# Optimization experiments

Hardware: AMD Instinct MI355X
Metric: run time of the kernel (lower is better)

Reference implementation:

```python
import jax, jax.numpy as jnp
import numpy as np

V = 1024      # token vocab
C = 8         # n_codebooks
T = 256       # seg_len
BP = 4        # block_pairs (n_latent_blocks)
K = 512       # latent_vocab_size (codebook entries)
E = 128       # emb_dim
D = 128       # latent_dim / d_model
BETA = 0.05
NB = 6 * BP   # decoder sequence length = 24
NH = 4
HD = D // NH
FF = 512
R = 8
IN_FLAT = NB * D
OUT = T * C * V
B = 32


def setup_inputs() -> dict:
    key = jax.random.key(0)
    ks = jax.random.split(key, 20)
    n = lambda i, shape, s=0.02: jax.random.normal(ks[i], shape, jnp.float32) * s
    return {
        "tokens_prev": jax.random.randint(ks[0], (B, T, C), 0, V, jnp.int32),
        "tokens_curr": jax.random.randint(ks[1], (B, T, C), 0, V, jnp.int32),
        "tokens_next": jax.random.randint(ks[2], (B, T, C), 0, V, jnp.int32),
        "emb": n(3, (V, E)),
        "conv1_w": n(4, (4 * D, E * C, 3)),
        "conv1_b": jnp.zeros((4 * D,), jnp.float32),
        "conv2_w": n(5, (2 * D, 4 * D, 1)),
        "conv2_b": jnp.zeros((2 * D,), jnp.float32),
        "cb_instru": jax.random.uniform(ks[6], (K, D), jnp.float32, -1.0 / K, 1.0 / K),
        "cb_vocal": jax.random.uniform(ks[7], (K, D), jnp.float32, -1.0 / K, 1.0 / K),
        "pos": n(8, (1, NB, D), 1.0),
        "attn_in_w": n(9, (3 * D, D)),
        "attn_in_b": jnp.zeros((3 * D,), jnp.float32),
        "attn_out_w": n(10, (D, D)),
        "attn_out_b": jnp.zeros((D,), jnp.float32),
        "ln1_g": jnp.ones((D,), jnp.float32),
        "ln1_b": jnp.zeros((D,), jnp.float32),
        "lin1_w": n(11, (FF, D)),
        "lin1_b": jnp.zeros((FF,), jnp.float32),
        "lin2_w": n(12, (D, FF)),
        "lin2_b": jnp.zeros((D,), jnp.float32),
        "ln2_g": jnp.ones((D,), jnp.float32),
        "ln2_b": jnp.zeros((D,), jnp.float32),
        "lora_a": n(13, (R, IN_FLAT), 0.01),
        "lora_b": n(14, (OUT, R), 0.01),
    }


def _conv1d(x, w, b, pad):
    # x: (B, Cin, L), w: (Cout, Cin, Kw)
    y = jax.lax.conv_general_dilated(x, w, window_strides=(1,), padding=[(pad, pad)],
                                     dimension_numbers=("NCH", "OIH", "NCH"))
    return y + b[None, :, None]


def _encode(tokens, emb, w1, b1, w2, b2):
    Bb, Tt, Cc = tokens.shape
    x = emb[tokens].reshape(Bb, Tt, -1).transpose(0, 2, 1)       # (B, C*E, T)
    x = jax.nn.relu(_conv1d(x, w1, b1, 1))                        # (B, 4D, T)
    x = jax.nn.relu(_conv1d(x, w2, b2, 0))                        # (B, 2D, T)
    # AdaptiveAvgPool1d(BP) with T % BP == 0 -> mean over contiguous chunks
    x = x.reshape(Bb, 2 * D, BP, Tt // BP).mean(-1).transpose(0, 2, 1)  # (B, BP, 2D)
    return x[..., :D], x[..., D:]


def _vq(z, codebook):
    # z: (B, N, D); eval-mode VQ (no EMA update)
    Bb, N, Dd = z.shape
    flat = z.reshape(-1, Dd)
    dist = (jnp.sum(flat * flat, axis=1, keepdims=True)
            - 2.0 * flat @ codebook.T
            + jnp.sum(codebook * codebook, axis=1))
    codes = jnp.argmin(dist, axis=1)
    z_q = codebook[codes].reshape(Bb, N, Dd)
    commit = jnp.mean((z - jax.lax.stop_gradient(z_q)) ** 2)
    loss = BETA * commit
    z_q_st = z + jax.lax.stop_gradient(z_q - z)
    return z_q_st, codes.reshape(Bb, N), loss


def _layer_norm(x, g, b):
    mu = x.mean(-1, keepdims=True)
    var = ((x - mu) ** 2).mean(-1, keepdims=True)
    return (x - mu) * jax.lax.rsqrt(var + 1e-5) * g + b


def _tf_layer(x, in_w, in_b, out_w, out_b, g1, b1, w1, bb1, w2, bb2, g2, b2):
    # Post-norm TransformerEncoderLayer (relu, eval/no-dropout). x: (B, S, D)
    Bb, S, Dd = x.shape
    qkv = x @ in_w.T + in_b
    q, k, v = jnp.split(qkv, 3, axis=-1)
    q = q.reshape(Bb, S, NH, HD).transpose(0, 2, 1, 3)
    k = k.reshape(Bb, S, NH, HD).transpose(0, 2, 1, 3)
    v = v.reshape(Bb, S, NH, HD).transpose(0, 2, 1, 3)
    attn = jax.nn.softmax(jnp.einsum("bhsd,bhtd->bhst", q, k) / np.sqrt(HD), axis=-1)
    o = jnp.einsum("bhst,bhtd->bhsd", attn, v).transpose(0, 2, 1, 3).reshape(Bb, S, Dd)
    x = _layer_norm(x + o @ out_w.T + out_b, g1, b1)
    ff = jax.nn.relu(x @ w1.T + bb1) @ w2.T + bb2
    return _layer_norm(x + ff, g2, b2)


def reference(tokens_prev, tokens_curr, tokens_next, emb, conv1_w, conv1_b,
              conv2_w, conv2_b, cb_instru, cb_vocal, pos, attn_in_w, attn_in_b,
              attn_out_w, attn_out_b, ln1_g, ln1_b, lin1_w, lin1_b, lin2_w,
              lin2_b, ln2_g, ln2_b, lora_a, lora_b):
    p_i, p_v = _encode(tokens_prev, emb, conv1_w, conv1_b, conv2_w, conv2_b)
    c_i, c_v = _encode(tokens_curr, emb, conv1_w, conv1_b, conv2_w, conv2_b)
    n_i, n_v = _encode(tokens_next, emb, conv1_w, conv1_b, conv2_w, conv2_b)
    p_i_q, _, l1 = _vq(p_i, cb_instru)
    c_i_q, _, l2 = _vq(c_i, cb_instru)
    n_i_q, _, l3 = _vq(n_i, cb_instru)
    p_v_q, _, l4 = _vq(p_v, cb_vocal)
    c_v_q, _, l5 = _vq(c_v, cb_vocal)
    n_v_q, _, l6 = _vq(n_v, cb_vocal)
    vq_loss = l1 + l2 + l3 + l4 + l5 + l6
    z = jnp.concatenate([p_i_q, p_v_q, c_i_q, c_v_q, n_i_q, n_v_q], axis=1)  # (B, 24, D)
    z = z + pos[:, :z.shape[1], :]
    z = _tf_layer(z, attn_in_w, attn_in_b, attn_out_w, attn_out_b,
                  ln1_g, ln1_b, lin1_w, lin1_b, lin2_w, lin2_b, ln2_g, ln2_b)
    Bb = z.shape[0]
    flat = z.reshape(Bb, -1)
    logits = (flat @ lora_a.T) @ lora_b.T          # (B, T*C*V)
    logits = logits.reshape(Bb, T, C, V)
    logp = jax.nn.log_softmax(logits, axis=-1)
    nll = -jnp.take_along_axis(logp, tokens_curr[..., None].astype(jnp.int32), axis=-1)
    recon_loss = nll.mean()
    total_loss = recon_loss + vq_loss
    return total_loss
```

## Files before the change

kernel.cpp:

```cpp
#include <hip/hip_runtime.h>
#include <hip/hip_bf16.h>
#include <cstdint>
#include <cstddef>

typedef __attribute__((ext_vector_type(8))) short short8;
typedef __attribute__((ext_vector_type(4))) float floatx4;


__device__ __forceinline__ ushort f2bf(float f) {
    union { float f; unsigned int u; } x; x.f = f;
    unsigned int r = (x.u + 0x7fffu + ((x.u >> 16) & 1u)) >> 16;
    return (ushort)r;
}
__device__ __forceinline__ float bf2f(ushort u) {
    union { unsigned int u; float f; } x; x.u = ((unsigned int)u) << 16;
    return x.f;
}

__global__ __launch_bounds__(256) void prep_all(
    const float* __restrict__ emb, const float* __restrict__ w1,
    const float* __restrict__ w2, const float* __restrict__ cbi,
    const float* __restrict__ cbv, const float* __restrict__ aiw,
    const float* __restrict__ aow, const float* __restrict__ l1w,
    const float* __restrict__ l2w,
    ushort* __restrict__ ebf, ushort* __restrict__ w1bf, ushort* __restrict__ w2bf,
    float* __restrict__ cbiT, float* __restrict__ cbvT,
    ushort* __restrict__ aiwbf, ushort* __restrict__ aowbf,
    ushort* __restrict__ l1wbf, ushort* __restrict__ l2wbf,
    float* __restrict__ accum)
{
    int idx = blockIdx.x * 256 + threadIdx.x;
    if (idx < 16) accum[idx] = 0.f;
    if (idx < 131072) {
        ebf[idx] = f2bf(emb[idx]);
    } else if (idx < 262144) {
        int j = idx - 131072; w2bf[j] = f2bf(w2[j]);
    } else if (idx < 327680) {
        int j = idx - 262144; cbiT[(j & 127) * 512 + (j >> 7)] = cbi[j];
    } else if (idx < 393216) {
        int j = idx - 327680; cbvT[(j & 127) * 512 + (j >> 7)] = cbv[j];
    } else if (idx < 442368) {
        int j = idx - 393216; aiwbf[j] = f2bf(aiw[j]);
    } else if (idx < 475136) {
        int j = idx - 442368; aowbf[j] = f2bf(aow[j]);
    } else if (idx < 540672) {
        int j = idx - 475136; l1wbf[j] = f2bf(l1w[j]);
    } else if (idx < 606208) {
        int j = idx - 540672; l2wbf[j] = f2bf(l2w[j]);
    } else if (idx < 1130496) {
        int j = idx - 606208;
        int e  = j & 127;
        int cc = (j >> 7) & 7;
        int co = j >> 10;
        const float* src = w1 + ((size_t)co * 1024 + cc * 128 + e) * 3;
        float v0 = src[0], v1 = src[1], v2 = src[2];
        w1bf[((size_t)(0 * 8 + cc) * 512 + co) * 128 + e] = f2bf(v0);
        w1bf[((size_t)(1 * 8 + cc) * 512 + co) * 128 + e] = f2bf(v1);
        w1bf[((size_t)(2 * 8 + cc) * 512 + co) * 128 + e] = f2bf(v2);
    }
}

__global__ __launch_bounds__(512, 4) void conv1_mfma(
    const int* __restrict__ tp, const int* __restrict__ tcu, const int* __restrict__ tn,
    const ushort* __restrict__ ebf, const ushort* __restrict__ w1bf,
    const float* __restrict__ b1, ushort* __restrict__ y1)
{
    constexpr int LDA = 136;
    __shared__ ushort As[130 * LDA];
    __shared__ ushort Bs[128 * LDA];
    __shared__ int tokL[130 * 8];
    const int tid = threadIdx.x;
    const int bx = blockIdx.x;
    const int nb = bx & 3, mb = bx >> 2;
    const int set = mb >> 6, rem = mb & 63, bb = rem >> 1, t0 = (rem & 1) << 7;
    const int n0 = nb << 7;
    const int* tok = (set == 0) ? tp : ((set == 1) ? tcu : tn);

    for (int idx = tid; idx < 1040; idx += 512) {
        const int row = idx >> 3, cc = idx & 7;
        const int gt = t0 + row - 1;
        tokL[idx] = (gt >= 0 && gt < 256) ? tok[bb * 2048 + gt * 8 + cc] : -1;
    }

    const int w = tid >> 6, lane = tid & 63;
    const int wm = w & 1, wn = w >> 1;
    const int rA = lane & 15, q4 = lane >> 4;
    const int ch = tid & 15, rowst = tid >> 4;

    floatx4 acc[4][2];
    for (int mi = 0; mi < 4; ++mi)
        for (int ni = 0; ni < 2; ++ni)
            acc[mi][ni] = (floatx4)(0.0f);

    __syncthreads();

    for (int cc = 0; cc < 8; ++cc) {
        for (int p = 0; p < 5; ++p) {
            const int row = p * 32 + rowst;
            if (row < 130) {
                const int tk = tokL[row * 8 + cc];
                uint4 val = make_uint4(0u, 0u, 0u, 0u);
                if (tk >= 0) val = *(const uint4*)(ebf + tk * 128 + ch * 8);
                *(uint4*)(As + row * LDA + ch * 8) = val;
            }
        }
        for (int kw = 0; kw < 3; ++kw) {
            const ushort* wsrc = w1bf + ((size_t)((kw * 8 + cc) * 512 + n0)) * 128;
            for (int p = 0; p < 4; ++p) {
                const int row = p * 32 + rowst;
                *(uint4*)(Bs + row * LDA + ch * 8) = *(const uint4*)(wsrc + row * 128 + ch * 8);
            }
            __syncthreads();
            for (int ks = 0; ks < 4; ++ks) {
                const int k0 = ks * 32 + q4 * 8;
                short8 a[4], bfr[2];
                for (int mi = 0; mi < 4; ++mi)
                    a[mi] = *(const short8*)(As + (wm * 64 + mi * 16 + rA + kw) * LDA + k0);
                for (int ni = 0; ni < 2; ++ni)
                    bfr[ni] = *(const short8*)(Bs + (wn * 32 + ni * 16 + rA) * LDA + k0);
                for (int mi = 0; mi < 4; ++mi)
                    for (int ni = 0; ni < 2; ++ni)
                        acc[mi][ni] = __builtin_amdgcn_mfma_f32_16x16x32_bf16(
                            a[mi], bfr[ni], acc[mi][ni], 0, 0, 0);
            }
            __syncthreads();
        }
    }
    for (int ni = 0; ni < 2; ++ni) {
        const int co = n0 + wn * 32 + ni * 16 + rA;
        const float bias = b1[co];
        for (int mi = 0; mi < 4; ++mi) {
            for (int r = 0; r < 4; ++r) {
                const int t = t0 + wm * 64 + mi * 16 + q4 * 4 + r;
                float v = acc[mi][ni][r] + bias;
                v = v > 0.f ? v : 0.f;
                y1[((size_t)(set * 32 + bb) * 256 + t) * 512 + co] = f2bf(v);
            }
        }
    }
}

__global__ __launch_bounds__(512, 4) void conv2_mfma(
    const ushort* __restrict__ y1, const ushort* __restrict__ w2bf,
    const float* __restrict__ b2, float* __restrict__ y2)
{
    constexpr int LDA = 136;
    __shared__ ushort As[128 * LDA];
    __shared__ ushort Bs[128 * LDA];
    __shared__ float pool[256];
    const int tid = threadIdx.x;
    const int bx = blockIdx.x;
    const int nb = bx & 1, mb = bx >> 1;
    const int set = mb >> 6, rem = mb & 63, bb = rem >> 1, t0 = (rem & 1) << 7;
    const int n0 = nb << 7;
    const int w = tid >> 6, lane = tid & 63;
    const int wm = w & 1, wn = w >> 1;
    const int rA = lane & 15, q4 = lane >> 4;
    const int ch = tid & 15, rowst = tid >> 4;

    floatx4 acc[4][2];
    for (int mi = 0; mi < 4; ++mi)
        for (int ni = 0; ni < 2; ++ni)
            acc[mi][ni] = (floatx4)(0.0f);

    const size_t arowbase = ((size_t)(set * 32 + bb) * 256 + t0) * 512;
    for (int kc = 0; kc < 4; ++kc) {
        for (int p = 0; p < 4; ++p) {
            const int row = p * 32 + rowst;
            *(uint4*)(As + row * LDA + ch * 8) =
                *(const uint4*)(y1 + arowbase + (size_t)row * 512 + kc * 128 + ch * 8);
            *(uint4*)(Bs + row * LDA + ch * 8) =
                *(const uint4*)(w2bf + (size_t)(n0 + row) * 512 + kc * 128 + ch * 8);
        }
        __syncthreads();
        for (int ks = 0; ks < 4; ++ks) {
            const int k0 = ks * 32 + q4 * 8;
            short8 a[4], bfr[2];
            for (int mi = 0; mi < 4; ++mi)
                a[mi] = *(const short8*)(As + (wm * 64 + mi * 16 + rA) * LDA + k0);
            for (int ni = 0; ni < 2; ++ni)
                bfr[ni] = *(const short8*)(Bs + (wn * 32 + ni * 16 + rA) * LDA + k0);
            for (int mi = 0; mi < 4; ++mi)
                for (int ni = 0; ni < 2; ++ni)
                    acc[mi][ni] = __builtin_amdgcn_mfma_f32_16x16x32_bf16(
                        a[mi], bfr[ni], acc[mi][ni], 0, 0, 0);
        }
        __syncthreads();
    }
    for (int ni = 0; ni < 2; ++ni) {
        const int col = wn * 32 + ni * 16 + rA;
        const float bias = b2[n0 + col];
        float s = 0.f;
        for (int mi = 0; mi < 4; ++mi)
            for (int r = 0; r < 4; ++r) {
                float v = acc[mi][ni][r] + bias;
                s += v > 0.f ? v : 0.f;
            }
        s += __shfl_xor(s, 16);
        s += __shfl_xor(s, 32);
        if (q4 == 0) pool[wm * 128 + col] = s;
    }
    __syncthreads();
    if (tid < 256) {
        const int wrow = tid >> 7, col = tid & 127;
        const int p = (t0 >> 6) + wrow;
        y2[((size_t)(set * 32 + bb) * 4 + p) * 256 + n0 + col] = pool[tid] * (1.f / 64.f);
    }
}

__global__ __launch_bounds__(256) void vq_kernel(
    const float* __restrict__ y2, const float* __restrict__ cbiT, const float* __restrict__ cbvT,
    const float* __restrict__ cbi, const float* __restrict__ cbv,
    const float* __restrict__ pos, float* __restrict__ ztr, float* __restrict__ accum)
{
    const int q = blockIdx.x;
    const int tid = threadIdx.x;
    const int set = q >> 7, bb = (q >> 2) & 31, p = q & 3;
    __shared__ float zloc[256];
    __shared__ float bestv[4];
    __shared__ int   besti[4];
    __shared__ int   code_sh[2];
    __shared__ float wsum2[4];
    zloc[tid] = y2[(size_t)q * 256 + tid];
    __syncthreads();
    const int w = tid >> 6, lane = tid & 63;
    const int half = w >> 1, sub = w & 1;
    const float4* cbT4 = (const float4*)(half ? cbvT : cbiT);
    const float* zh = zloc + half * 128;
    const int k4 = sub * 64 + lane;
    float a0 = 0.f, a1 = 0.f, a2 = 0.f, a3 = 0.f;
    for (int d = 0; d < 128; ++d) {
        float4 v = cbT4[d * 128 + k4];
        const float z = zh[d];
        float d0 = z - v.x, d1 = z - v.y, d2 = z - v.z, d3 = z - v.w;
        a0 += d0 * d0; a1 += d1 * d1; a2 += d2 * d2; a3 += d3 * d3;
    }
    float best = a0; int bidx = k4 * 4;
    if (a1 < best) { best = a1; bidx = k4 * 4 + 1; }
    if (a2 < best) { best = a2; bidx = k4 * 4 + 2; }
    if (a3 < best) { best = a3; bidx = k4 * 4 + 3; }
    for (int off = 32; off > 0; off >>= 1) {
        float ov = __shfl_xor(best, off);
        int   oi = __shfl_xor(bidx, off);
        if (ov < best || (ov == best && oi < bidx)) { best = ov; bidx = oi; }
    }
    if (lane == 0) { bestv[w] = best; besti[w] = bidx; }
    __syncthreads();
    if (tid < 2) {
        float v0 = bestv[tid * 2], v1 = bestv[tid * 2 + 1];
        int   i0 = besti[tid * 2], i1 = besti[tid * 2 + 1];
        code_sh[tid] = (v1 < v0 || (v1 == v0 && i1 < i0)) ? i1 : i0;
    }
    __syncthreads();
    const int hh = tid >> 7, d = tid & 127;
    const int code = code_sh[hh];
    const float* cb = hh ? cbv : cbi;
    const float zq = cb[code * 128 + d];
    const float diff = zloc[hh * 128 + d] - zq;
    float sq = diff * diff;
    for (int off = 32; off > 0; off >>= 1) sq += __shfl_xor(sq, off);
    if (lane == 0) wsum2[w] = sq;
    const int s = (set * 2 + hh) * 4 + p;
    ztr[((size_t)bb * 24 + s) * 128 + d] = zq + pos[s * 128 + d];
    __syncthreads();
    if (tid == 0) atomicAdd(&accum[0], wsum2[0] + wsum2[1] + wsum2[2] + wsum2[3]);
}

__global__ __launch_bounds__(1024) void tail_kernel(
    const float* __restrict__ ztr,
    const ushort* __restrict__ aiwbf, const float* __restrict__ aib,
    const ushort* __restrict__ aowbf, const float* __restrict__ aob,
    const float* __restrict__ g1, const float* __restrict__ be1,
    const ushort* __restrict__ l1wbf, const float* __restrict__ l1b,
    const ushort* __restrict__ l2wbf, const float* __restrict__ l2b,
    const float* __restrict__ g2, const float* __restrict__ be2,
    const float* __restrict__ lora_a, float* __restrict__ hbuf)
{
    __shared__ __align__(16) char LDSC[162304];
    float*  Xf  = (float*)LDSC;
    ushort* Abf = (ushort*)(LDSC + 12288);
    char*   S   = LDSC + 20992;
    ushort* Wq  = (ushort*)S;
    float*  QKV = (float*)(S + 104448);
    float*  Ssc = (float*)S;
    ushort* Wo  = (ushort*)S;
    float*  psA = (float*)(S + 36864);
    float*  pqA = (float*)(S + 37888);
    float*  muvA= (float*)(S + 38912);
    float*  invA= (float*)(S + 39040);
    ushort* W1  = (ushort*)S;
    ushort* Hbf = (ushort*)S;
    ushort* Wh  = (ushort*)(S + 33280);
    float*  psB = (float*)(S + 100864);
    float*  pqB = (float*)(S + 101888);
    float*  muvB= (float*)(S + 102912);
    float*  invB= (float*)(S + 103040);
    float*  psL = (float*)(S + 103168);

    const int b = blockIdx.x;
    const int tid = threadIdx.x;
    const int w = tid >> 6, lane = tid & 63;
    const int rA = lane & 15, q4 = lane >> 4;
    const int ch = tid & 15;

    if (tid < 544) ((uint4*)Abf)[tid] = make_uint4(0u, 0u, 0u, 0u);
    __syncthreads();
    for (int i = tid; i < 3072; i += 1024) {
        float v = ztr[(size_t)b * 3072 + i];
        Xf[i] = v;
        Abf[(i >> 7) * 136 + (i & 127)] = f2bf(v);
    }
    for (int i = tid; i < 6144; i += 1024) {
        const int row = i >> 4, c = i & 15;
        *(uint4*)(Wq + row * 136 + c * 8) = *(const uint4*)(aiwbf + row * 128 + c * 8);
    }
    __syncthreads();

    {
        floatx4 acc[3];
        int mI[3], nI[3];
        for (int i = 0; i < 3; ++i) {
            const int t = w + 16 * i;
            mI[i] = t / 24; nI[i] = t % 24;
            acc[i] = (floatx4)(0.f);
        }
        for (int ks = 0; ks < 4; ++ks) {
            const int k0 = ks * 32 + q4 * 8;
            for (int i = 0; i < 3; ++i) {
                short8 a = *(const short8*)(Abf + (mI[i] * 16 + rA) * 136 + k0);
                short8 bf = *(const short8*)(Wq + (nI[i] * 16 + rA) * 136 + k0);
                acc[i] = __builtin_amdgcn_mfma_f32_16x16x32_bf16(a, bf, acc[i], 0, 0, 0);
            }
        }
        for (int i = 0; i < 3; ++i) {
            const int col = nI[i] * 16 + rA;
            const float bs = aib[col];
            for (int r = 0; r < 4; ++r) {
                const int row = mI[i] * 16 + q4 * 4 + r;
                if (row < 24) QKV[row * 384 + col] = acc[i][r] + bs;
            }
        }
    }
    __syncthreads();

    for (int it = 0; it < 3; ++it) {
        const int e = it * 1024 + tid;
        if (e < 2304) {
            const int h = e / 576, rem = e % 576, i = rem / 24, j = rem % 24;
            float s = 0.f;
            for (int d = 0; d < 32; ++d)
                s += QKV[i * 384 + h * 32 + d] * QKV[j * 384 + 128 + h * 32 + d];
            Ssc[h * 576 + i * 24 + j] = s * 0.17677669529663687f;
        }
    }
    __syncthreads();
    if (tid < 96) {
        const int h = tid / 24, r = tid % 24;
        float* row = Ssc + h * 576 + r * 24;
        float m = row[0];
        for (int j = 1; j < 24; ++j) m = row[j] > m ? row[j] : m;
        float ssum = 0.f;
        for (int j = 0; j < 24; ++j) { float e = __expf(row[j] - m); row[j] = e; ssum += e; }
        float iv = 1.f / ssum;
        for (int j = 0; j < 24; ++j) row[j] *= iv;
    }
    __syncthreads();
    for (int it = 0; it < 3; ++it) {
        const int idx = it * 1024 + tid;
        const int s = idx >> 7, dcol = idx & 127, h = dcol >> 5, d = dcol & 31;
        if (s < 24) {
            float a = 0.f;
            for (int j = 0; j < 24; ++j)
                a += Ssc[h * 576 + s * 24 + j] * QKV[j * 384 + 256 + h * 32 + d];
            Abf[s * 136 + dcol] = f2bf(a);
        }
    }
    __syncthreads();

    for (int i = tid; i < 2048; i += 1024) {
        const int row = i >> 4, c = i & 15;
        *(uint4*)(Wo + row * 136 + c * 8) = *(const uint4*)(aowbf + row * 128 + c * 8);
    }
    __syncthreads();

    {
        const int m = w & 1, n = w >> 1;
        floatx4 acc = (floatx4)(0.f);
        for (int ks = 0; ks < 4; ++ks) {
            const int k0 = ks * 32 + q4 * 8;
            short8 a = *(const short8*)(Abf + (m * 16 + rA) * 136 + k0);
            short8 bf = *(const short8*)(Wo + (n * 16 + rA) * 136 + k0);
            acc = __builtin_amdgcn_mfma_f32_16x16x32_bf16(a, bf, acc, 0, 0, 0);
        }
        const int col = n * 16 + rA;
        const float bs = aob[col];
        for (int r = 0; r < 4; ++r) {
            const int row = m * 16 + q4 * 4 + r;
            acc[r] += bs + (row < 24 ? Xf[row * 128 + col] : 0.f);
        }
        float s4 = 0.f, q4s = 0.f;
        for (int r = 0; r < 4; ++r) {
            float s = acc[r], sq = acc[r] * acc[r];
            for (int off = 1; off < 16; off <<= 1) { s += __shfl_xor(s, off); sq += __shfl_xor(sq, off); }
            if (rA == 0) {
                const int rl = m * 16 + q4 * 4 + r;
                psA[rl * 8 + n] = s; pqA[rl * 8 + n] = sq;
            }
        }
        (void)s4; (void)q4s;
        __syncthreads();
        if (tid < 32) {
            float s = 0.f, sq = 0.f;
            for (int j = 0; j < 8; ++j) { s += psA[tid * 8 + j]; sq += pqA[tid * 8 + j]; }
            float mu = s * (1.f / 128.f);
            float var = sq * (1.f / 128.f) - mu * mu;
            muvA[tid] = mu; invA[tid] = rsqrtf(var + 1e-5f);
        }
        __syncthreads();
        const float gg = g1[col], bb2 = be1[col];
        for (int r = 0; r < 4; ++r) {
            const int rl = m * 16 + q4 * 4 + r;
            if (rl < 24) {
                float v = (acc[r] - muvA[rl]) * invA[rl] * gg + bb2;
                Xf[rl * 128 + col] = v;
                Abf[rl * 136 + col] = f2bf(v);
            }
        }
    }
    __syncthreads();

    for (int i = tid; i < 8192; i += 1024) {
        const int row = i >> 4, c = i & 15;
        *(uint4*)(W1 + row * 136 + c * 8) = *(const uint4*)(l1wbf + row * 128 + c * 8);
    }
    __syncthreads();

    {
        const int m = w & 1, n0b = w >> 1;
        floatx4 acc[4];
        for (int i = 0; i < 4; ++i) acc[i] = (floatx4)(0.f);
        for (int ks = 0; ks < 4; ++ks) {
            const int k0 = ks * 32 + q4 * 8;
            short8 a = *(const short8*)(Abf + (m * 16 + rA) * 136 + k0);
            for (int i = 0; i < 4; ++i) {
                const int n = n0b + i * 8;
                short8 bf = *(const short8*)(W1 + (n * 16 + rA) * 136 + k0);
                acc[i] = __builtin_amdgcn_mfma_f32_16x16x32_bf16(a, bf, acc[i], 0, 0, 0);
            }
        }
        __syncthreads();
        for (int i = 0; i < 4; ++i) {
            const int col = (n0b + i * 8) * 16 + rA;
            const float bs = l1b[col];
            for (int r = 0; r < 4; ++r) {
                const int row = m * 16 + q4 * 4 + r;
                if (row < 24) {
                    float v = acc[i][r] + bs;
                    Hbf[row * 520 + col] = f2bf(v > 0.f ? v : 0.f);
                }
            }
        }
    }
    __syncthreads();

    {
        const int m = w & 1, n = w >> 1;
        floatx4 acc = (floatx4)(0.f);
        for (int kh = 0; kh < 2; ++kh) {
            if (kh) __syncthreads();
            for (int i = tid; i < 4096; i += 1024) {
                const int row = i >> 5, c = i & 31;
                *(uint4*)(Wh + row * 264 + c * 8) =
                    *(const uint4*)(l2wbf + row * 512 + kh * 256 + c * 8);
            }
            __syncthreads();
            for (int ks = 0; ks < 8; ++ks) {
                const int k0 = ks * 32 + q4 * 8;
                short8 a = *(const short8*)(Hbf + (m * 16 + rA) * 520 + kh * 256 + k0);
                short8 bf = *(const short8*)(Wh + (n * 16 + rA) * 264 + k0);
                acc = __builtin_amdgcn_mfma_f32_16x16x32_bf16(a, bf, acc, 0, 0, 0);
            }
        }
        const int col = n * 16 + rA;
        const float bs = l2b[col];
        for (int r = 0; r < 4; ++r) {
            const int row = m * 16 + q4 * 4 + r;
            acc[r] += bs + (row < 24 ? Xf[row * 128 + col] : 0.f);
        }
        for (int r = 0; r < 4; ++r) {
            float s = acc[r], sq = acc[r] * acc[r];
            for (int off = 1; off < 16; off <<= 1) { s += __shfl_xor(s, off); sq += __shfl_xor(sq, off); }
            if (rA == 0) {
                const int rl = m * 16 + q4 * 4 + r;
                psB[rl * 8 + n] = s; pqB[rl * 8 + n] = sq;
            }
        }
        __syncthreads();
        if (tid < 32) {
            float s = 0.f, sq = 0.f;
            for (int j = 0; j < 8; ++j) { s += psB[tid * 8 + j]; sq += pqB[tid * 8 + j]; }
            float mu = s * (1.f / 128.f);
            float var = sq * (1.f / 128.f) - mu * mu;
            muvB[tid] = mu; invB[tid] = rsqrtf(var + 1e-5f);
        }
        __syncthreads();
        const float gg = g2[col], bb2 = be2[col];
        for (int r = 0; r < 4; ++r) {
            const int rl = m * 16 + q4 * 4 + r;
            if (rl < 24)
                Xf[rl * 128 + col] = (acc[r] - muvB[rl]) * invB[rl] * gg + bb2;
        }
    }
    __syncthreads();

    {
        const int r = w & 7, seg = w >> 3;
        float a = 0.f;
        for (int k = 0; k < 24; ++k) {
            const int idx = seg * 1536 + k * 64 + lane;
            a += lora_a[(size_t)r * 3072 + idx] * Xf[idx];
        }
        for (int off = 32; off > 0; off >>= 1) a += __shfl_xor(a, off);
        if (lane == 0) psL[r * 2 + seg] = a;
        __syncthreads();
        if (tid < 8) hbuf[b * 8 + tid] = psL[tid * 2] + psL[tid * 2 + 1];
    }
}

__global__ __launch_bounds__(256) void logits_kernel(
    const float* __restrict__ hbuf, const float* __restrict__ lora_b,
    const int* __restrict__ tokc, float* __restrict__ accum, float* __restrict__ out)
{
    const int tid = threadIdx.x;
    const int tcb = blockIdx.x;
    __shared__ float hl[256];
    __shared__ float wsum[4];
    __shared__ float ltok;
    hl[tid] = hbuf[tid];
    float wr[4][8];
    for (int i = 0; i < 4; ++i) {
        const float4* pw = (const float4*)(lora_b + ((size_t)tcb * 1024 + tid + 256 * i) * 8);
        float4 x = pw[0], y = pw[1];
        wr[i][0] = x.x; wr[i][1] = x.y; wr[i][2] = x.z; wr[i][3] = x.w;
        wr[i][4] = y.x; wr[i][5] = y.y; wr[i][6] = y.z; wr[i][7] = y.w;
    }
    __syncthreads();
    float nll = 0.f;
    for (int bb = 0; bb < 32; ++bb) {
        const int tv = tokc[bb * 2048 + tcb];
        const float* h = hl + bb * 8;
        float h0 = h[0], h1 = h[1], h2 = h[2], h3 = h[3];
        float h4 = h[4], h5 = h[5], h6 = h[6], h7 = h[7];
        float sl = 0.f;
        for (int i = 0; i < 4; ++i) {
            float lg = h0 * wr[i][0] + h1 * wr[i][1] + h2 * wr[i][2] + h3 * wr[i][3]
                     + h4 * wr[i][4] + h5 * wr[i][5] + h6 * wr[i][6] + h7 * wr[i][7];
            sl += __expf(lg);
            if (tid + 256 * i == tv) ltok = lg;
        }
        for (int off = 32; off > 0; off >>= 1) sl += __shfl_xor(sl, off);
        if ((tid & 63) == 0) wsum[tid >> 6] = sl;
        __syncthreads();
        if (tid == 0) nll += logf(wsum[0] + wsum[1] + wsum[2] + wsum[3]) - ltok;
        __syncthreads();
    }
    if (tid == 0) {
        atomicAdd(&accum[1], nll);
        __threadfence();
        unsigned int prev = atomicAdd((unsigned int*)(accum + 2), 1u);
        if (prev == 2047u) {
            float vq  = atomicAdd(&accum[0], 0.f);
            float rec = atomicAdd(&accum[1], 0.f);
            out[0] = rec * (1.f / 65536.f) + 0.05f * vq * (1.f / 16384.f);
        }
    }
}

extern "C" void kernel_launch(void* const* d_in, const int* in_sizes, int n_in,
                              void* d_out, int out_size, void* d_ws, size_t ws_size,
                              hipStream_t stream) {
    const int*   tp   = (const int*)d_in[0];
    const int*   tcu  = (const int*)d_in[1];
    const int*   tn   = (const int*)d_in[2];
    const float* emb  = (const float*)d_in[3];
    const float* w1   = (const float*)d_in[4];
    const float* b1   = (const float*)d_in[5];
    const float* w2   = (const float*)d_in[6];
    const float* b2   = (const float*)d_in[7];
    const float* cbi  = (const float*)d_in[8];
    const float* cbv  = (const float*)d_in[9];
    const float* pos  = (const float*)d_in[10];
    const float* aiw  = (const float*)d_in[11];
    const float* aib  = (const float*)d_in[12];
    const float* aow  = (const float*)d_in[13];
    const float* aob  = (const float*)d_in[14];
    const float* g1   = (const float*)d_in[15];
    const float* be1  = (const float*)d_in[16];
    const float* l1w  = (const float*)d_in[17];
    const float* l1b  = (const float*)d_in[18];
    const float* l2w  = (const float*)d_in[19];
    const float* l2b  = (const float*)d_in[20];
    const float* g2   = (const float*)d_in[21];
    const float* be2  = (const float*)d_in[22];
    const float* lra  = (const float*)d_in[23];
    const float* lrb  = (const float*)d_in[24];

    char* wsb = (char*)d_ws;
    ushort* ebf  = (ushort*)(wsb + 0);
    ushort* w1bf = (ushort*)(wsb + 262144);
    ushort* w2bf = (ushort*)(wsb + 3407872);
    float*  cbiT = (float*)(wsb + 3670016);
    float*  cbvT = (float*)(wsb + 3932160);
    ushort* y1   = (ushort*)(wsb + 4194304);
    float*  y2   = (float*)(wsb + 29360128);
    float*  ztr  = (float*)(wsb + 29753344);
    float*  hbuf = (float*)(wsb + 30146560);
    float*  accum= (float*)(wsb + 30147584);
    ushort* aiwbf= (ushort*)(wsb + 30147648);
    ushort* aowbf= (ushort*)(wsb + 30245952);
    ushort* l1wbf= (ushort*)(wsb + 30278720);
    ushort* l2wbf= (ushort*)(wsb + 30409792);
    if (ws_size < 30540864) return;

    prep_all<<<4416, 256, 0, stream>>>(emb, w1, w2, cbi, cbv, aiw, aow, l1w, l2w,
                                       ebf, w1bf, w2bf, cbiT, cbvT,
                                       aiwbf, aowbf, l1wbf, l2wbf, accum);
    conv1_mfma<<<768, 512, 0, stream>>>(tp, tcu, tn, ebf, w1bf, b1, y1);
    conv2_mfma<<<384, 512, 0, stream>>>(y1, w2bf, b2, y2);
    vq_kernel<<<384, 256, 0, stream>>>(y2, cbiT, cbvT, cbi, cbv, pos, ztr, accum);
    tail_kernel<<<32, 1024, 0, stream>>>(ztr, aiwbf, aib, aowbf, aob, g1, be1,
                                         l1wbf, l1b, l2wbf, l2b, g2, be2, lra, hbuf);
    logits_kernel<<<2048, 256, 0, stream>>>(hbuf, lrb, tcu, accum, (float*)d_out);
}
```

Before: 361.0 us.

## Shrink conv1 M-tile to 64 rows, hold tokens in registers, batch logits reductions

conv1 now tiles 64 time steps per block instead of 128, which doubles the grid. It raises the occupancy hint to 6, shrinks the shared-memory A tile, and keeps the token indices in per-thread registers instead of a shared table. The logits kernel stages the per-batch target tokens in shared memory and stores per-wave partial sums for all 32 batch rows. It then reduces once at the end, removing two block barriers per batch iteration. The smaller conv1 tile means more weight (B) tile reloads per output and more halo overhead, in exchange for better latency hiding.

Result: slower. 387.8 us (+7.4%).

```diff
diff --git a/kernel.cpp b/kernel.cpp
--- a/kernel.cpp
+++ b/kernel.cpp
@@ -60,45 +60,45 @@
     }
 }
 
-__global__ __launch_bounds__(512, 4) void conv1_mfma(
+__global__ __launch_bounds__(512, 6) void conv1_mfma(
     const int* __restrict__ tp, const int* __restrict__ tcu, const int* __restrict__ tn,
     const ushort* __restrict__ ebf, const ushort* __restrict__ w1bf,
     const float* __restrict__ b1, ushort* __restrict__ y1)
 {
     constexpr int LDA = 136;
-    __shared__ ushort As[130 * LDA];
+    __shared__ ushort As[66 * LDA];
     __shared__ ushort Bs[128 * LDA];
-    __shared__ int tokL[130 * 8];
     const int tid = threadIdx.x;
     const int bx = blockIdx.x;
     const int nb = bx & 3, mb = bx >> 2;
-    const int set = mb >> 6, rem = mb & 63, bb = rem >> 1, t0 = (rem & 1) << 7;
+    const int set = mb >> 7, bb = (mb >> 2) & 31, t0 = (mb & 3) << 6;
     const int n0 = nb << 7;
     const int* tok = (set == 0) ? tp : ((set == 1) ? tcu : tn);
-
-    for (int idx = tid; idx < 1040; idx += 512) {
-        const int row = idx >> 3, cc = idx & 7;
-        const int gt = t0 + row - 1;
-        tokL[idx] = (gt >= 0 && gt < 256) ? tok[bb * 2048 + gt * 8 + cc] : -1;
-    }
 
     const int w = tid >> 6, lane = tid & 63;
     const int wm = w & 1, wn = w >> 1;
     const int rA = lane & 15, q4 = lane >> 4;
     const int ch = tid & 15, rowst = tid >> 4;
 
-    floatx4 acc[4][2];
-    for (int mi = 0; mi < 4; ++mi)
+    int tokr[3][8];
+    for (int p = 0; p < 3; ++p) {
+        const int row = p * 32 + rowst;
+        const int gt = t0 + row - 1;
+        const bool ok = (row < 66) && (gt >= 0) && (gt < 256);
+        for (int cc = 0; cc < 8; ++cc)
+            tokr[p][cc] = ok ? tok[bb * 2048 + gt * 8 + cc] : -1;
+    }
+
+    floatx4 acc[2][2];
+    for (int mi = 0; mi < 2; ++mi)
         for (int ni = 0; ni < 2; ++ni)
             acc[mi][ni] = (floatx4)(0.0f);
 
-    __syncthreads();
-
     for (int cc = 0; cc < 8; ++cc) {
-        for (int p = 0; p < 5; ++p) {
+        for (int p = 0; p < 3; ++p) {
             const int row = p * 32 + rowst;
-            if (row < 130) {
-                const int tk = tokL[row * 8 + cc];
+            if (row < 66) {
+                const int tk = tokr[p][cc];
                 uint4 val = make_uint4(0u, 0u, 0u, 0u);
                 if (tk >= 0) val = *(const uint4*)(ebf + tk * 128 + ch * 8);
                 *(uint4*)(As + row * LDA + ch * 8) = val;
@@ -113,12 +113,12 @@
             __syncthreads();
             for (int ks = 0; ks < 4; ++ks) {
                 const int k0 = ks * 32 + q4 * 8;
-                short8 a[4], bfr[2];
-                for (int mi = 0; mi < 4; ++mi)
-                    a[mi] = *(const short8*)(As + (wm * 64 + mi * 16 + rA + kw) * LDA + k0);
+                short8 a[2], bfr[2];
+                for (int mi = 0; mi < 2; ++mi)
+                    a[mi] = *(const short8*)(As + (wm * 32 + mi * 16 + rA + kw) * LDA + k0);
                 for (int ni = 0; ni < 2; ++ni)
                     bfr[ni] = *(const short8*)(Bs + (wn * 32 + ni * 16 + rA) * LDA + k0);
-                for (int mi = 0; mi < 4; ++mi)
+                for (int mi = 0; mi < 2; ++mi)
                     for (int ni = 0; ni < 2; ++ni)
                         acc[mi][ni] = __builtin_amdgcn_mfma_f32_16x16x32_bf16(
                             a[mi], bfr[ni], acc[mi][ni], 0, 0, 0);
@@ -129,9 +129,9 @@
     for (int ni = 0; ni < 2; ++ni) {
         const int co = n0 + wn * 32 + ni * 16 + rA;
         const float bias = b1[co];
-        for (int mi = 0; mi < 4; ++mi) {
+        for (int mi = 0; mi < 2; ++mi) {
             for (int r = 0; r < 4; ++r) {
-                const int t = t0 + wm * 64 + mi * 16 + q4 * 4 + r;
+                const int t = t0 + wm * 32 + mi * 16 + q4 * 4 + r;
                 float v = acc[mi][ni][r] + bias;
                 v = v > 0.f ? v : 0.f;
                 y1[((size_t)(set * 32 + bb) * 256 + t) * 512 + co] = f2bf(v);
@@ -301,7 +301,6 @@
     const int tid = threadIdx.x;
     const int w = tid >> 6, lane = tid & 63;
     const int rA = lane & 15, q4 = lane >> 4;
-    const int ch = tid & 15;
 
     if (tid < 544) ((uint4*)Abf)[tid] = make_uint4(0u, 0u, 0u, 0u);
     __syncthreads();
@@ -398,7 +397,6 @@
             const int row = m * 16 + q4 * 4 + r;
             acc[r] += bs + (row < 24 ? Xf[row * 128 + col] : 0.f);
         }
-        float s4 = 0.f, q4s = 0.f;
         for (int r = 0; r < 4; ++r) {
             float s = acc[r], sq = acc[r] * acc[r];
             for (int off = 1; off < 16; off <<= 1) { s += __shfl_xor(s, off); sq += __shfl_xor(sq, off); }
@@ -407,7 +405,6 @@
                 psA[rl * 8 + n] = s; pqA[rl * 8 + n] = sq;
             }
         }
-        (void)s4; (void)q4s;
         __syncthreads();
         if (tid < 32) {
             float s = 0.f, sq = 0.f;
@@ -533,21 +530,24 @@
 {
     const int tid = threadIdx.x;
     const int tcb = blockIdx.x;
+    const int w = tid >> 6, lane = tid & 63;
     __shared__ float hl[256];
-    __shared__ float wsum[4];
-    __shared__ float ltok;
+    __shared__ float slsum[32][4];
+    __shared__ float ltokL[32];
+    __shared__ int   tvL[32];
     hl[tid] = hbuf[tid];
+    if (tid < 32) tvL[tid] = tokc[tid * 2048 + tcb];
     float wr[4][8];
     for (int i = 0; i < 4; ++i) {
-        const float4* pw = (const float4*)(lora_b + ((size_t)tcb * 1024 + tid + 256 * i) * 8);
+        const int vidx = w * 256 + i * 64 + lane;
+        const float4* pw = (const float4*)(lora_b + ((size_t)tcb * 1024 + vidx) * 8);
         float4 x = pw[0], y = pw[1];
         wr[i][0] = x.x; wr[i][1] = x.y; wr[i][2] = x.z; wr[i][3] = x.w;
         wr[i][4] = y.x; wr[i][5] = y.y; wr[i][6] = y.z; wr[i][7] = y.w;
     }
     __syncthreads();
-    float nll = 0.f;
     for (int bb = 0; bb < 32; ++bb) {
-        const int tv = tokc[bb * 2048 + tcb];
+        const int tv = tvL[bb];
         const float* h = hl + bb * 8;
         float h0 = h[0], h1 = h[1], h2 = h[2], h3 = h[3];
         float h4 = h[4], h5 = h[5], h6 = h[6], h7 = h[7];
@@ -556,22 +556,26 @@
             float lg = h0 * wr[i][0] + h1 * wr[i][1] + h2 * wr[i][2] + h3 * wr[i][3]
                      + h4 * wr[i][4] + h5 * wr[i][5] + h6 * wr[i][6] + h7 * wr[i][7];
             sl += __expf(lg);
-            if (tid + 256 * i == tv) ltok = lg;
+            if (w * 256 + i * 64 + lane == tv) ltokL[bb] = lg;
         }
         for (int off = 32; off > 0; off >>= 1) sl += __shfl_xor(sl, off);
-        if ((tid & 63) == 0) wsum[tid >> 6] = sl;
-        __syncthreads();
-        if (tid == 0) nll += logf(wsum[0] + wsum[1] + wsum[2] + wsum[3]) - ltok;
-        __syncthreads();
-    }
-    if (tid == 0) {
-        atomicAdd(&accum[1], nll);
-        __threadfence();
-        unsigned int prev = atomicAdd((unsigned int*)(accum + 2), 1u);
-        if (prev == 2047u) {
-            float vq  = atomicAdd(&accum[0], 0.f);
-            float rec = atomicAdd(&accum[1], 0.f);
-            out[0] = rec * (1.f / 65536.f) + 0.05f * vq * (1.f / 16384.f);
+        if (lane == 0) slsum[bb][w] = sl;
+    }
+    __syncthreads();
+    float nll = 0.f;
+    if (tid < 32)
+        nll = logf(slsum[tid][0] + slsum[tid][1] + slsum[tid][2] + slsum[tid][3]) - ltokL[tid];
+    if (tid < 64) {
+        for (int off = 32; off > 0; off >>= 1) nll += __shfl_xor(nll, off);
+        if (tid == 0) {
+            atomicAdd(&accum[1], nll);
+            __threadfence();
+            unsigned int prev = atomicAdd((unsigned int*)(accum + 2), 1u);
+            if (prev == 2047u) {
+                float vq  = atomicAdd(&accum[0], 0.f);
+                float rec = atomicAdd(&accum[1], 0.f);
+                out[0] = rec * (1.f / 65536.f) + 0.05f * vq * (1.f / 16384.f);
+            }
         }
     }
 }
@@ -625,7 +629,7 @@
     prep_all<<<4416, 256, 0, stream>>>(emb, w1, w2, cbi, cbv, aiw, aow, l1w, l2w,
                                        ebf, w1bf, w2bf, cbiT, cbvT,
                                        aiwbf, aowbf, l1wbf, l2wbf, accum);
-    conv1_mfma<<<768, 512, 0, stream>>>(tp, tcu, tn, ebf, w1bf, b1, y1);
+    conv1_mfma<<<1536, 512, 0, stream>>>(tp, tcu, tn, ebf, w1bf, b1, y1);
     conv2_mfma<<<384, 512, 0, stream>>>(y1, w2bf, b2, y2);
     vq_kernel<<<384, 256, 0, stream>>>(y2, cbiT, cbvT, cbi, cbv, pos, ztr, accum);
     tail_kernel<<<32, 1024, 0, stream>>>(ztr, aiwbf, aib, aowbf, aob, g1, be1,
```

## Use direct global-to-LDS loads in conv1 and batch logits reductions

Applied to the files above, without the earlier changes.

The conv1 kernel now fills its shared-memory A and B tiles with global_load_lds DMA-style loads instead of staging through registers, with a zeroed pad buffer standing in for out-of-range tokens. The tiles lose their padded row stride, which may add LDS bank conflicts on the MFMA fragment reads. Separately, the logits kernel caches target tokens in shared memory and defers the per-batch block reductions into a single pass, removing 64 barriers per block.

After: 474.7 us. +31.5%, slower.

```diff
diff --git a/kernel.cpp b/kernel.cpp
--- a/kernel.cpp
+++ b/kernel.cpp
@@ -15,6 +15,12 @@
 __device__ __forceinline__ float bf2f(ushort u) {
     union { unsigned int u; float f; } x; x.u = ((unsigned int)u) << 16;
     return x.f;
+}
+
+__device__ __forceinline__ void gl_lds16(const void* g, void* l) {
+    __builtin_amdgcn_global_load_lds(
+        (const __attribute__((address_space(1))) void*)g,
+        (__attribute__((address_space(3))) void*)l, 16, 0, 0);
 }
 
 __global__ __launch_bounds__(256) void prep_all(
@@ -27,10 +33,11 @@
     float* __restrict__ cbiT, float* __restrict__ cbvT,
     ushort* __restrict__ aiwbf, ushort* __restrict__ aowbf,
     ushort* __restrict__ l1wbf, ushort* __restrict__ l2wbf,
-    float* __restrict__ accum)
+    float* __restrict__ accum, ushort* __restrict__ zpad)
 {
     int idx = blockIdx.x * 256 + threadIdx.x;
     if (idx < 16) accum[idx] = 0.f;
+    if (idx < 128) zpad[idx] = 0;
     if (idx < 131072) {
         ebf[idx] = f2bf(emb[idx]);
     } else if (idx < 262144) {
@@ -63,11 +70,11 @@
 __global__ __launch_bounds__(512, 4) void conv1_mfma(
     const int* __restrict__ tp, const int* __restrict__ tcu, const int* __restrict__ tn,
     const ushort* __restrict__ ebf, const ushort* __restrict__ w1bf,
-    const float* __restrict__ b1, ushort* __restrict__ y1)
+    const float* __restrict__ b1, const ushort* __restrict__ zpad,
+    ushort* __restrict__ y1)
 {
-    constexpr int LDA = 136;
-    __shared__ ushort As[130 * LDA];
-    __shared__ ushort Bs[128 * LDA];
+    __shared__ ushort As[130 * 128];
+    __shared__ ushort Bs[128 * 128];
     __shared__ int tokL[130 * 8];
     const int tid = threadIdx.x;
     const int bx = blockIdx.x;
@@ -99,25 +106,24 @@
             const int row = p * 32 + rowst;
             if (row < 130) {
                 const int tk = tokL[row * 8 + cc];
-                uint4 val = make_uint4(0u, 0u, 0u, 0u);
-                if (tk >= 0) val = *(const uint4*)(ebf + tk * 128 + ch * 8);
-                *(uint4*)(As + row * LDA + ch * 8) = val;
+                const ushort* src = (tk >= 0) ? (ebf + (size_t)tk * 128 + ch * 8)
+                                              : (zpad + ch * 8);
+                gl_lds16(src, As + (p * 32 + w * 4) * 128);
             }
         }
         for (int kw = 0; kw < 3; ++kw) {
             const ushort* wsrc = w1bf + ((size_t)((kw * 8 + cc) * 512 + n0)) * 128;
-            for (int p = 0; p < 4; ++p) {
-                const int row = p * 32 + rowst;
-                *(uint4*)(Bs + row * LDA + ch * 8) = *(const uint4*)(wsrc + row * 128 + ch * 8);
-            }
+            for (int p = 0; p < 4; ++p)
+                gl_lds16(wsrc + (p * 32 + rowst) * 128 + ch * 8,
+                         Bs + (p * 32 + w * 4) * 128);
             __syncthreads();
             for (int ks = 0; ks < 4; ++ks) {
                 const int k0 = ks * 32 + q4 * 8;
                 short8 a[4], bfr[2];
                 for (int mi = 0; mi < 4; ++mi)
-                    a[mi] = *(const short8*)(As + (wm * 64 + mi * 16 + rA + kw) * LDA + k0);
+                    a[mi] = *(const short8*)(As + (wm * 64 + mi * 16 + rA + kw) * 128 + k0);
                 for (int ni = 0; ni < 2; ++ni)
-                    bfr[ni] = *(const short8*)(Bs + (wn * 32 + ni * 16 + rA) * LDA + k0);
+                    bfr[ni] = *(const short8*)(Bs + (wn * 32 + ni * 16 + rA) * 128 + k0);
                 for (int mi = 0; mi < 4; ++mi)
                     for (int ni = 0; ni < 2; ++ni)
                         acc[mi][ni] = __builtin_amdgcn_mfma_f32_16x16x32_bf16(
@@ -301,7 +307,6 @@
     const int tid = threadIdx.x;
     const int w = tid >> 6, lane = tid & 63;
     const int rA = lane & 15, q4 = lane >> 4;
-    const int ch = tid & 15;
 
     if (tid < 544) ((uint4*)Abf)[tid] = make_uint4(0u, 0u, 0u, 0u);
     __syncthreads();
@@ -398,7 +403,6 @@
             const int row = m * 16 + q4 * 4 + r;
             acc[r] += bs + (row < 24 ? Xf[row * 128 + col] : 0.f);
         }
-        float s4 = 0.f, q4s = 0.f;
         for (int r = 0; r < 4; ++r) {
             float s = acc[r], sq = acc[r] * acc[r];
             for (int off = 1; off < 16; off <<= 1) { s += __shfl_xor(s, off); sq += __shfl_xor(sq, off); }
@@ -407,7 +411,6 @@
                 psA[rl * 8 + n] = s; pqA[rl * 8 + n] = sq;
             }
         }
-        (void)s4; (void)q4s;
         __syncthreads();
         if (tid < 32) {
             float s = 0.f, sq = 0.f;
@@ -533,21 +536,24 @@
 {
     const int tid = threadIdx.x;
     const int tcb = blockIdx.x;
+    const int w = tid >> 6, lane = tid & 63;
     __shared__ float hl[256];
-    __shared__ float wsum[4];
-    __shared__ float ltok;
+    __shared__ float slsum[32][4];
+    __shared__ float ltokL[32];
+    __shared__ int   tvL[32];
     hl[tid] = hbuf[tid];
+    if (tid < 32) tvL[tid] = tokc[tid * 2048 + tcb];
     float wr[4][8];
     for (int i = 0; i < 4; ++i) {
-        const float4* pw = (const float4*)(lora_b + ((size_t)tcb * 1024 + tid + 256 * i) * 8);
+        const int vidx = w * 256 + i * 64 + lane;
+        const float4* pw = (const float4*)(lora_b + ((size_t)tcb * 1024 + vidx) * 8);
         float4 x = pw[0], y = pw[1];
         wr[i][0] = x.x; wr[i][1] = x.y; wr[i][2] = x.z; wr[i][3] = x.w;
         wr[i][4] = y.x; wr[i][5] = y.y; wr[i][6] = y.z; wr[i][7] = y.w;
     }
     __syncthreads();
-    float nll = 0.f;
     for (int bb = 0; bb < 32; ++bb) {
-        const int tv = tokc[bb * 2048 + tcb];
+        const int tv = tvL[bb];
         const float* h = hl + bb * 8;
         float h0 = h[0], h1 = h[1], h2 = h[2], h3 = h[3];
         float h4 = h[4], h5 = h[5], h6 = h[6], h7 = h[7];
@@ -556,22 +562,26 @@
             float lg = h0 * wr[i][0] + h1 * wr[i][1] + h2 * wr[i][2] + h3 * wr[i][3]
                      + h4 * wr[i][4] + h5 * wr[i][5] + h6 * wr[i][6] + h7 * wr[i][7];
             sl += __expf(lg);
-            if (tid + 256 * i == tv) ltok = lg;
+            if (w * 256 + i * 64 + lane == tv) ltokL[bb] = lg;
         }
         for (int off = 32; off > 0; off >>= 1) sl += __shfl_xor(sl, off);
-        if ((tid & 63) == 0) wsum[tid >> 6] = sl;
-        __syncthreads();
-        if (tid == 0) nll += logf(wsum[0] + wsum[1] + wsum[2] + wsum[3]) - ltok;
-        __syncthreads();
-    }
-    if (tid == 0) {
-        atomicAdd(&accum[1], nll);
-        __threadfence();
-        unsigned int prev = atomicAdd((unsigned int*)(accum + 2), 1u);
-        if (prev == 2047u) {
-            float vq  = atomicAdd(&accum[0], 0.f);
-            float rec = atomicAdd(&accum[1], 0.f);
-            out[0] = rec * (1.f / 65536.f) + 0.05f * vq * (1.f / 16384.f);
+        if (lane == 0) slsum[bb][w] = sl;
+    }
+    __syncthreads();
+    float nll = 0.f;
+    if (tid < 32)
+        nll = logf(slsum[tid][0] + slsum[tid][1] + slsum[tid][2] + slsum[tid][3]) - ltokL[tid];
+    if (tid < 64) {
+        for (int off = 32; off > 0; off >>= 1) nll += __shfl_xor(nll, off);
+        if (tid == 0) {
+            atomicAdd(&accum[1], nll);
+            __threadfence();
+            unsigned int prev = atomicAdd((unsigned int*)(accum + 2), 1u);
+            if (prev == 2047u) {
+                float vq  = atomicAdd(&accum[0], 0.f);
+                float rec = atomicAdd(&accum[1], 0.f);
+                out[0] = rec * (1.f / 65536.f) + 0.05f * vq * (1.f / 16384.f);
+            }
         }
     }
 }
@@ -620,12 +630,13 @@
     ushort* aowbf= (ushort*)(wsb + 30245952);
     ushort* l1wbf= (ushort*)(wsb + 30278720);
     ushort* l2wbf= (ushort*)(wsb + 30409792);
-    if (ws_size < 30540864) return;
+    ushort* zpad = (ushort*)(wsb + 30540864);
+    if (ws_size < 30541120) return;
 
     prep_all<<<4416, 256, 0, stream>>>(emb, w1, w2, cbi, cbv, aiw, aow, l1w, l2w,
                                        ebf, w1bf, w2bf, cbiT, cbvT,
-                                       aiwbf, aowbf, l1wbf, l2wbf, accum);
-    conv1_mfma<<<768, 512, 0, stream>>>(tp, tcu, tn, ebf, w1bf, b1, y1);
+                                       aiwbf, aowbf, l1wbf, l2wbf, accum, zpad);
+    conv1_mfma<<<768, 512, 0, stream>>>(tp, tcu, tn, ebf, w1bf, b1, zpad, y1);
     conv2_mfma<<<384, 512, 0, stream>>>(y1, w2bf, b2, y2);
     vq_kernel<<<384, 256, 0, stream>>>(y2, cbiT, cbvT, cbi, cbv, pos, ztr, accum);
     tail_kernel<<<32, 1024, 0, stream>>>(ztr, aiwbf, aib, aowbf, aob, g1, be1,
```
